# Kernel optimization log

Hardware: AMD Instinct MI355X
Metric: run time of the kernel (lower is better)

## Reference

```python
import jax, jax.numpy as jnp
import numpy as np

ALPHA = 20.0 / 100.0  # dt / tau
ONE_MINUS_ALPHA = 1.0 - ALPHA


def setup_inputs() -> dict:
    key = jax.random.key(0)
    ks = jax.random.split(key, 5)
    seq_len, batch, input_size, hidden_size = 512, 256, 64, 256
    x = jax.random.normal(ks[0], (seq_len, batch, input_size), dtype=jnp.float32)
    hidden = jnp.zeros((batch, hidden_size), dtype=jnp.float32)
    # per-step noise, shape (seq_len, hidden_size); broadcast over batch like torch.normal(std*ones(H))
    noise_seq = jax.random.normal(ks[1], (seq_len, hidden_size), dtype=jnp.float32)
    # small init scale keeps the leaky-relu recurrence stable over 512 steps
    W_in = jax.random.normal(ks[2], (hidden_size, input_size), dtype=jnp.float32) * 0.05
    b_in = jnp.zeros((hidden_size,), dtype=jnp.float32)
    W_hh = jax.random.normal(ks[3], (hidden_size, hidden_size), dtype=jnp.float32) * 0.05
    b_hh = jnp.zeros((hidden_size,), dtype=jnp.float32)
    return {"x": x, "hidden": hidden, "noise_seq": noise_seq,
            "W_in": W_in, "b_in": b_in, "W_hh": W_hh, "b_hh": b_hh}


def reference(x, hidden, noise_seq, W_in, b_in, W_hh, b_hh):
    # x: [T, B, I]; hidden: [B, H]; noise_seq: [T, H]
    def step(h, inp):
        xt, nt = inp  # xt: [B, I], nt: [H]
        pre = xt @ W_in.T + b_in + h @ W_hh.T + b_hh + nt
        h_new = jnp.maximum(h * ONE_MINUS_ALPHA + pre * ALPHA, 0.0)
        return h_new, h_new
    h_last, out = jax.lax.scan(step, hidden, (x, noise_seq))
    return out, h_last  # out: [T, B, H]
```

## Files before the change

### kernel.cpp

```cpp
#include <hip/hip_runtime.h>


#define T_STEPS 512
#define BATCH   256
#define INSZ    64
#define HID     256
#define ALPHA_F 0.2f
#define OMA_F   0.8f

__global__ __launch_bounds__(512, 2)
void ctrnn_prex(const float* __restrict__ x,
                const float* __restrict__ noise,
                const float* __restrict__ W_in,
                const float* __restrict__ b_in,
                const float* __restrict__ b_hh,
                float* __restrict__ prex)
{
    const int tid = threadIdx.x;
    const int j   = tid & (HID - 1);
    const int g   = tid >> 8;

    __shared__ __align__(16) float xs[2][2][INSZ];

    float win[INSZ];
#pragma unroll
    for (int k = 0; k < INSZ; k += 4) {
        float4 v = *reinterpret_cast<const float4*>(&W_in[j * INSZ + k]);
        win[k] = v.x; win[k+1] = v.y; win[k+2] = v.z; win[k+3] = v.w;
    }
    const float bias = b_in[j] + b_hh[j];

    const int base = blockIdx.x * 256;
    if (j < INSZ / 4) {
        *reinterpret_cast<float4*>(&xs[0][g][4 * j]) =
            *reinterpret_cast<const float4*>(&x[(size_t)(base + g) * INSZ + 4 * j]);
    }
    __syncthreads();

    int cur = 0;
#pragma unroll 1
    for (int i = 0; i < 128; ++i) {
        const int p = base + 2 * i + g;
        if (i + 1 < 128 && j < INSZ / 4) {
            *reinterpret_cast<float4*>(&xs[cur ^ 1][g][4 * j]) =
                *reinterpret_cast<const float4*>(
                    &x[(size_t)(p + 2) * INSZ + 4 * j]);
        }
        const int t = p >> 8;
        const float nz = noise[t * HID + j];

        float a0 = 0.f, a1 = 0.f, a2 = 0.f, a3 = 0.f;
#pragma unroll
        for (int k = 0; k < INSZ; k += 4) {
            float4 xv = *reinterpret_cast<const float4*>(&xs[cur][g][k]);
            a0 = fmaf(win[k],     xv.x, a0);
            a1 = fmaf(win[k + 1], xv.y, a1);
            a2 = fmaf(win[k + 2], xv.z, a2);
            a3 = fmaf(win[k + 3], xv.w, a3);
        }
        prex[(size_t)p * HID + j] = (a0 + a1) + (a2 + a3) + bias + nz;
        __syncthreads();
        cur ^= 1;
    }
}

__global__ __launch_bounds__(1024, 4)
void ctrnn_rec(const float* __restrict__ hidden,
               const float* __restrict__ prex,
               const float* __restrict__ W_hh,
               float* __restrict__ out)
{
    const int tid = threadIdx.x;
    const int jj  = tid & 63;
    const int g   = tid >> 6;
    const int b   = blockIdx.x;

    __shared__ __align__(16) float hbuf[2][HID];
    __shared__ __align__(16) float pbuf[16][HID];

    float w[4][16];
#pragma unroll
    for (int m = 0; m < 4; ++m) {
        const float* wrow = &W_hh[(jj + 64 * m) * HID + 16 * g];
#pragma unroll
        for (int c = 0; c < 4; ++c) {
            float4 v = *reinterpret_cast<const float4*>(&wrow[4 * c]);
            w[m][4*c]   = v.x; w[m][4*c+1] = v.y;
            w[m][4*c+2] = v.z; w[m][4*c+3] = v.w;
        }
    }

    float hj = 0.f, pcur = 0.f, pn1 = 0.f;
    if (tid < HID) {
        hj = hidden[b * HID + tid];
        hbuf[0][tid] = hj;
        pcur = prex[(size_t)b * HID + tid];
        pn1  = prex[((size_t)1 * BATCH + b) * HID + tid];
    }
    __syncthreads();

    const int koff = 16 * g;
    int cur = 0;
#pragma unroll 1
    for (int t = 0; t < T_STEPS; ++t) {
        float pn2 = 0.f;
        if (tid < HID && t + 2 < T_STEPS) {
            pn2 = prex[((size_t)(t + 2) * BATCH + b) * HID + tid];
        }

        float4 h0 = *reinterpret_cast<const float4*>(&hbuf[cur][koff]);
        float4 h1 = *reinterpret_cast<const float4*>(&hbuf[cur][koff + 4]);
        float4 h2 = *reinterpret_cast<const float4*>(&hbuf[cur][koff + 8]);
        float4 h3 = *reinterpret_cast<const float4*>(&hbuf[cur][koff + 12]);

        float acc[4];
#pragma unroll
        for (int m = 0; m < 4; ++m) {
            float a = 0.f, bq = 0.f;
            a  = fmaf(w[m][0],  h0.x, a);  bq = fmaf(w[m][1],  h0.y, bq);
            a  = fmaf(w[m][2],  h0.z, a);  bq = fmaf(w[m][3],  h0.w, bq);
            a  = fmaf(w[m][4],  h1.x, a);  bq = fmaf(w[m][5],  h1.y, bq);
            a  = fmaf(w[m][6],  h1.z, a);  bq = fmaf(w[m][7],  h1.w, bq);
            a  = fmaf(w[m][8],  h2.x, a);  bq = fmaf(w[m][9],  h2.y, bq);
            a  = fmaf(w[m][10], h2.z, a);  bq = fmaf(w[m][11], h2.w, bq);
            a  = fmaf(w[m][12], h3.x, a);  bq = fmaf(w[m][13], h3.y, bq);
            a  = fmaf(w[m][14], h3.z, a);  bq = fmaf(w[m][15], h3.w, bq);
            acc[m] = a + bq;
        }
        pbuf[g][jj]       = acc[0];
        pbuf[g][jj + 64]  = acc[1];
        pbuf[g][jj + 128] = acc[2];
        pbuf[g][jj + 192] = acc[3];
        __syncthreads();

        const int nxt = cur ^ 1;
        if (tid < HID) {
            float s = pcur;
#pragma unroll
            for (int gg = 0; gg < 16; ++gg) s += pbuf[gg][tid];
            hj = fmaxf(fmaf(OMA_F, hj, ALPHA_F * s), 0.f);
            out[((size_t)t * BATCH + b) * HID + tid] = hj;
            hbuf[nxt][tid] = hj;
            pcur = pn1; pn1 = pn2;
        }
        __syncthreads();
        cur = nxt;
    }

    if (tid < HID) {
        out[(size_t)T_STEPS * BATCH * HID + (size_t)b * HID + tid] = hj;
    }
}

__global__ __launch_bounds__(512, 2)
void ctrnn_mono(const float* __restrict__ x, const float* __restrict__ hidden,
                const float* __restrict__ noise, const float* __restrict__ W_in,
                const float* __restrict__ b_in, const float* __restrict__ W_hh,
                const float* __restrict__ b_hh, float* __restrict__ out)
{
    const int tid  = threadIdx.x;
    const int j    = tid & (HID - 1);
    const int half = tid >> 8;
    const int b    = blockIdx.x;

    __shared__ __align__(16) float hbuf[2][HID];
    __shared__ __align__(16) float xbuf[2][INSZ];
    __shared__ __align__(16) float pbuf[HID];

    float whh[128];
    const float* wrow = &W_hh[j * HID + half * 128];
#pragma unroll
    for (int k = 0; k < 128; k += 4) {
        float4 v = *reinterpret_cast<const float4*>(&wrow[k]);
        whh[k] = v.x; whh[k+1] = v.y; whh[k+2] = v.z; whh[k+3] = v.w;
    }
    float win[32];
    const float* wirow = &W_in[j * INSZ + half * 32];
#pragma unroll
    for (int k = 0; k < 32; k += 4) {
        float4 v = *reinterpret_cast<const float4*>(&wirow[k]);
        win[k] = v.x; win[k+1] = v.y; win[k+2] = v.z; win[k+3] = v.w;
    }

    float bias = 0.f, hj = 0.f, noise_j = 0.f;
    if (half == 0) {
        bias = b_in[j] + b_hh[j];
        hj = hidden[b * HID + j];
        hbuf[0][j] = hj;
        noise_j = noise[j];
        if (j < INSZ / 4) {
            *reinterpret_cast<float4*>(&xbuf[0][4 * j]) =
                *reinterpret_cast<const float4*>(&x[(size_t)b * INSZ + 4 * j]);
        }
    }
    __syncthreads();

    const int hoff = half * 128;
    const int ioff = half * 32;
    int cur = 0;
#pragma unroll 1
    for (int t = 0; t < T_STEPS; ++t) {
        float4 xnext = make_float4(0.f, 0.f, 0.f, 0.f);
        float  nnext = 0.f;
        if (half == 1) {
            if (j < INSZ / 4 && t + 1 < T_STEPS) {
                xnext = *reinterpret_cast<const float4*>(
                    &x[((size_t)(t + 1) * BATCH + b) * INSZ + 4 * j]);
            }
        } else if (t + 1 < T_STEPS) {
            nnext = noise[(t + 1) * HID + j];
        }

        float a0 = 0.f, a1 = 0.f, a2 = 0.f, a3 = 0.f;
#pragma unroll
        for (int k = 0; k < 128; k += 4) {
            float4 hv = *reinterpret_cast<const float4*>(&hbuf[cur][hoff + k]);
            a0 = fmaf(whh[k],     hv.x, a0);
            a1 = fmaf(whh[k + 1], hv.y, a1);
            a2 = fmaf(whh[k + 2], hv.z, a2);
            a3 = fmaf(whh[k + 3], hv.w, a3);
        }
#pragma unroll
        for (int k = 0; k < 32; k += 4) {
            float4 xv = *reinterpret_cast<const float4*>(&xbuf[cur][ioff + k]);
            a0 = fmaf(win[k],     xv.x, a0);
            a1 = fmaf(win[k + 1], xv.y, a1);
            a2 = fmaf(win[k + 2], xv.z, a2);
            a3 = fmaf(win[k + 3], xv.w, a3);
        }
        const float acc = (a0 + a1) + (a2 + a3);

        if (half == 1) pbuf[j] = acc;
        __syncthreads();

        const int nxt = cur ^ 1;
        if (half == 0) {
            const float pre = acc + pbuf[j] + bias + noise_j;
            hj = fmaxf(fmaf(OMA_F, hj, ALPHA_F * pre), 0.f);
            out[((size_t)t * BATCH + b) * HID + j] = hj;
            hbuf[nxt][j] = hj;
            noise_j = nnext;
        } else if (j < INSZ / 4 && t + 1 < T_STEPS) {
            *reinterpret_cast<float4*>(&xbuf[nxt][4 * j]) = xnext;
        }
        __syncthreads();
        cur = nxt;
    }

    if (half == 0) {
        out[(size_t)T_STEPS * BATCH * HID + (size_t)b * HID + j] = hj;
    }
}

extern "C" void kernel_launch(void* const* d_in, const int* in_sizes, int n_in,
                              void* d_out, int out_size, void* d_ws, size_t ws_size,
                              hipStream_t stream) {
    const float* x      = (const float*)d_in[0];
    const float* hidden = (const float*)d_in[1];
    const float* noise  = (const float*)d_in[2];
    const float* W_in   = (const float*)d_in[3];
    const float* b_in   = (const float*)d_in[4];
    const float* W_hh   = (const float*)d_in[5];
    const float* b_hh   = (const float*)d_in[6];
    float* out = (float*)d_out;

    const size_t prex_bytes = (size_t)T_STEPS * BATCH * HID * sizeof(float);
    if (ws_size >= prex_bytes) {
        float* prex = (float*)d_ws;
        hipLaunchKernelGGL(ctrnn_prex, dim3(512), dim3(512), 0, stream,
                           x, noise, W_in, b_in, b_hh, prex);
        hipLaunchKernelGGL(ctrnn_rec, dim3(BATCH), dim3(1024), 0, stream,
                           hidden, prex, W_hh, out);
    } else {
        hipLaunchKernelGGL(ctrnn_mono, dim3(BATCH), dim3(512), 0, stream,
                           x, hidden, noise, W_in, b_in, W_hh, b_hh, out);
    }
}
```

Baseline: 613.4 us.

## Fuse input projection into recurrent kernel with single barrier per step

Drops the separate input-projection kernel and its 128MB workspace round trip, folding the W_in·x product into the per-step recurrent matvec. Each 16-wide group handles 4 input columns alongside its W_hh slice. The reduction is spread across all threads with shuffles, and the partial-sum buffer is double-buffered so each timestep needs one raw s_barrier instead of two __syncthreads. The hidden-state buffer is now single, and its correctness depends on barrier ordering. That adds more per-step work inside the serial loop in exchange for removing global memory traffic.

```diff
diff --git a/kernel.cpp b/kernel.cpp
--- a/kernel.cpp
+++ b/kernel.cpp
@@ -8,247 +8,124 @@
 #define ALPHA_F 0.2f
 #define OMA_F   0.8f
 
-__global__ __launch_bounds__(512, 2)
-void ctrnn_prex(const float* __restrict__ x,
-                const float* __restrict__ noise,
-                const float* __restrict__ W_in,
-                const float* __restrict__ b_in,
-                const float* __restrict__ b_hh,
-                float* __restrict__ prex)
+__global__ __launch_bounds__(1024, 4)
+void ctrnn_fused(const float* __restrict__ x,
+                 const float* __restrict__ hidden,
+                 const float* __restrict__ noise,
+                 const float* __restrict__ W_in,
+                 const float* __restrict__ b_in,
+                 const float* __restrict__ W_hh,
+                 const float* __restrict__ b_hh,
+                 float* __restrict__ out)
 {
-    const int tid = threadIdx.x;
-    const int j   = tid & (HID - 1);
-    const int g   = tid >> 8;
+    const int tid  = threadIdx.x;
+    const int lane = tid & 63;
+    const int g    = tid >> 6;
+    const int b    = blockIdx.x;
 
-    __shared__ __align__(16) float xs[2][2][INSZ];
-
-    float win[INSZ];
-#pragma unroll
-    for (int k = 0; k < INSZ; k += 4) {
-        float4 v = *reinterpret_cast<const float4*>(&W_in[j * INSZ + k]);
-        win[k] = v.x; win[k+1] = v.y; win[k+2] = v.z; win[k+3] = v.w;
-    }
-    const float bias = b_in[j] + b_hh[j];
-
-    const int base = blockIdx.x * 256;
-    if (j < INSZ / 4) {
-        *reinterpret_cast<float4*>(&xs[0][g][4 * j]) =
-            *reinterpret_cast<const float4*>(&x[(size_t)(base + g) * INSZ + 4 * j]);
-    }
-    __syncthreads();
-
-    int cur = 0;
-#pragma unroll 1
-    for (int i = 0; i < 128; ++i) {
-        const int p = base + 2 * i + g;
-        if (i + 1 < 128 && j < INSZ / 4) {
-            *reinterpret_cast<float4*>(&xs[cur ^ 1][g][4 * j]) =
-                *reinterpret_cast<const float4*>(
-                    &x[(size_t)(p + 2) * INSZ + 4 * j]);
-        }
-        const int t = p >> 8;
-        const float nz = noise[t * HID + j];
-
-        float a0 = 0.f, a1 = 0.f, a2 = 0.f, a3 = 0.f;
-#pragma unroll
-        for (int k = 0; k < INSZ; k += 4) {
-            float4 xv = *reinterpret_cast<const float4*>(&xs[cur][g][k]);
-            a0 = fmaf(win[k],     xv.x, a0);
-            a1 = fmaf(win[k + 1], xv.y, a1);
-            a2 = fmaf(win[k + 2], xv.z, a2);
-            a3 = fmaf(win[k + 3], xv.w, a3);
-        }
-        prex[(size_t)p * HID + j] = (a0 + a1) + (a2 + a3) + bias + nz;
-        __syncthreads();
-        cur ^= 1;
-    }
-}
-
-__global__ __launch_bounds__(1024, 4)
-void ctrnn_rec(const float* __restrict__ hidden,
-               const float* __restrict__ prex,
-               const float* __restrict__ W_hh,
-               float* __restrict__ out)
-{
-    const int tid = threadIdx.x;
-    const int jj  = tid & 63;
-    const int g   = tid >> 6;
-    const int b   = blockIdx.x;
-
-    __shared__ __align__(16) float hbuf[2][HID];
-    __shared__ __align__(16) float pbuf[16][HID];
+    __shared__ __align__(16) float xbuf[2][INSZ];
+    __shared__ __align__(16) float hbuf[HID];
+    __shared__ __align__(16) float pbuf[2][16 * 264];
 
     float w[4][16];
 #pragma unroll
     for (int m = 0; m < 4; ++m) {
-        const float* wrow = &W_hh[(jj + 64 * m) * HID + 16 * g];
+        const float* wr = &W_hh[(lane + 64 * m) * HID + 16 * g];
 #pragma unroll
         for (int c = 0; c < 4; ++c) {
-            float4 v = *reinterpret_cast<const float4*>(&wrow[4 * c]);
+            float4 v = *reinterpret_cast<const float4*>(&wr[4 * c]);
             w[m][4*c]   = v.x; w[m][4*c+1] = v.y;
             w[m][4*c+2] = v.z; w[m][4*c+3] = v.w;
         }
     }
+    float wi[4][4];
+#pragma unroll
+    for (int m = 0; m < 4; ++m) {
+        float4 v = *reinterpret_cast<const float4*>(
+            &W_in[(lane + 64 * m) * INSZ + 4 * g]);
+        wi[m][0] = v.x; wi[m][1] = v.y; wi[m][2] = v.z; wi[m][3] = v.w;
+    }
 
-    float hj = 0.f, pcur = 0.f, pn1 = 0.f;
-    if (tid < HID) {
-        hj = hidden[b * HID + tid];
-        hbuf[0][tid] = hj;
-        pcur = prex[(size_t)b * HID + tid];
-        pn1  = prex[((size_t)1 * BATCH + b) * HID + tid];
+    const int rrow = 16 * g + (lane & 15);
+    const float biasl = b_in[rrow] + b_hh[rrow];
+    float hj  = hidden[b * HID + rrow];
+    float nn0 = noise[rrow];
+    float nn1 = noise[HID + rrow];
+
+    float4 xr = make_float4(0.f, 0.f, 0.f, 0.f);
+    if (g == 0 && lane < 16) {
+        *reinterpret_cast<float4*>(&xbuf[0][4 * lane]) =
+            *reinterpret_cast<const float4*>(&x[(size_t)b * INSZ + 4 * lane]);
+        xr = *reinterpret_cast<const float4*>(
+            &x[((size_t)BATCH + b) * INSZ + 4 * lane]);
     }
+    if (lane < 16) hbuf[rrow] = hj;
     __syncthreads();
 
-    const int koff = 16 * g;
-    int cur = 0;
+    const int redoff = ((g >> 2) << 6) + ((g & 3) << 4) + (lane & 15);
+    const int q = lane >> 4;
+
 #pragma unroll 1
     for (int t = 0; t < T_STEPS; ++t) {
-        float pn2 = 0.f;
-        if (tid < HID && t + 2 < T_STEPS) {
-            pn2 = prex[((size_t)(t + 2) * BATCH + b) * HID + tid];
+        const int cur = t & 1;
+
+        float nn2 = 0.f;
+        if (t + 2 < T_STEPS) nn2 = noise[(t + 2) * HID + rrow];
+        if (g == 0 && lane < 16) {
+            *reinterpret_cast<float4*>(&xbuf[cur ^ 1][4 * lane]) = xr;
+            if (t + 2 < T_STEPS)
+                xr = *reinterpret_cast<const float4*>(
+                    &x[((size_t)(t + 2) * BATCH + b) * INSZ + 4 * lane]);
         }
 
-        float4 h0 = *reinterpret_cast<const float4*>(&hbuf[cur][koff]);
-        float4 h1 = *reinterpret_cast<const float4*>(&hbuf[cur][koff + 4]);
-        float4 h2 = *reinterpret_cast<const float4*>(&hbuf[cur][koff + 8]);
-        float4 h3 = *reinterpret_cast<const float4*>(&hbuf[cur][koff + 12]);
+        const float4 h0 = *reinterpret_cast<const float4*>(&hbuf[16 * g]);
+        const float4 h1 = *reinterpret_cast<const float4*>(&hbuf[16 * g + 4]);
+        const float4 h2 = *reinterpret_cast<const float4*>(&hbuf[16 * g + 8]);
+        const float4 h3 = *reinterpret_cast<const float4*>(&hbuf[16 * g + 12]);
+        const float4 xv = *reinterpret_cast<const float4*>(&xbuf[cur][4 * g]);
 
-        float acc[4];
+        float accs[4];
 #pragma unroll
         for (int m = 0; m < 4; ++m) {
-            float a = 0.f, bq = 0.f;
-            a  = fmaf(w[m][0],  h0.x, a);  bq = fmaf(w[m][1],  h0.y, bq);
+            float a  = w[m][0] * h0.x;
+            float bq = w[m][1] * h0.y;
+            float cc = wi[m][0] * xv.x;
+            float dd = wi[m][1] * xv.y;
             a  = fmaf(w[m][2],  h0.z, a);  bq = fmaf(w[m][3],  h0.w, bq);
+            cc = fmaf(wi[m][2], xv.z, cc); dd = fmaf(wi[m][3], xv.w, dd);
             a  = fmaf(w[m][4],  h1.x, a);  bq = fmaf(w[m][5],  h1.y, bq);
             a  = fmaf(w[m][6],  h1.z, a);  bq = fmaf(w[m][7],  h1.w, bq);
             a  = fmaf(w[m][8],  h2.x, a);  bq = fmaf(w[m][9],  h2.y, bq);
             a  = fmaf(w[m][10], h2.z, a);  bq = fmaf(w[m][11], h2.w, bq);
             a  = fmaf(w[m][12], h3.x, a);  bq = fmaf(w[m][13], h3.y, bq);
             a  = fmaf(w[m][14], h3.z, a);  bq = fmaf(w[m][15], h3.w, bq);
-            acc[m] = a + bq;
+            accs[m] = (a + bq) + (cc + dd);
         }
-        pbuf[g][jj]       = acc[0];
-        pbuf[g][jj + 64]  = acc[1];
-        pbuf[g][jj + 128] = acc[2];
-        pbuf[g][jj + 192] = acc[3];
-        __syncthreads();
 
-        const int nxt = cur ^ 1;
-        if (tid < HID) {
-            float s = pcur;
-#pragma unroll
-            for (int gg = 0; gg < 16; ++gg) s += pbuf[gg][tid];
-            hj = fmaxf(fmaf(OMA_F, hj, ALPHA_F * s), 0.f);
-            out[((size_t)t * BATCH + b) * HID + tid] = hj;
-            hbuf[nxt][tid] = hj;
-            pcur = pn1; pn1 = pn2;
+        float* pb = &pbuf[cur][g * 264 + lane];
+        pb[0]   = accs[0];
+        pb[64]  = accs[1];
+        pb[128] = accs[2];
+        pb[192] = accs[3];
+
+        asm volatile("s_waitcnt lgkmcnt(0)\n\ts_barrier" ::: "memory");
+
+        const float* pr = &pbuf[cur][q * 264 + redoff];
+        float s = (pr[0] + pr[1056]) + (pr[2112] + pr[3168]);
+        s += __shfl_xor(s, 16);
+        s += __shfl_xor(s, 32);
+
+        const float pre = s + biasl + nn0;
+        hj = fmaxf(fmaf(OMA_F, hj, ALPHA_F * pre), 0.f);
+        if (lane < 16) {
+            out[((size_t)t * BATCH + b) * HID + rrow] = hj;
+            hbuf[rrow] = hj;
         }
-        __syncthreads();
-        cur = nxt;
+        nn0 = nn1; nn1 = nn2;
     }
 
-    if (tid < HID) {
-        out[(size_t)T_STEPS * BATCH * HID + (size_t)b * HID + tid] = hj;
-    }
-}
-
-__global__ __launch_bounds__(512, 2)
-void ctrnn_mono(const float* __restrict__ x, const float* __restrict__ hidden,
-                const float* __restrict__ noise, const float* __restrict__ W_in,
-                const float* __restrict__ b_in, const float* __restrict__ W_hh,
-                const float* __restrict__ b_hh, float* __restrict__ out)
-{
-    const int tid  = threadIdx.x;
-    const int j    = tid & (HID - 1);
-    const int half = tid >> 8;
-    const int b    = blockIdx.x;
-
-    __shared__ __align__(16) float hbuf[2][HID];
-    __shared__ __align__(16) float xbuf[2][INSZ];
-    __shared__ __align__(16) float pbuf[HID];
-
-    float whh[128];
-    const float* wrow = &W_hh[j * HID + half * 128];
-#pragma unroll
-    for (int k = 0; k < 128; k += 4) {
-        float4 v = *reinterpret_cast<const float4*>(&wrow[k]);
-        whh[k] = v.x; whh[k+1] = v.y; whh[k+2] = v.z; whh[k+3] = v.w;
-    }
-    float win[32];
-    const float* wirow = &W_in[j * INSZ + half * 32];
-#pragma unroll
-    for (int k = 0; k < 32; k += 4) {
-        float4 v = *reinterpret_cast<const float4*>(&wirow[k]);
-        win[k] = v.x; win[k+1] = v.y; win[k+2] = v.z; win[k+3] = v.w;
-    }
-
-    float bias = 0.f, hj = 0.f, noise_j = 0.f;
-    if (half == 0) {
-        bias = b_in[j] + b_hh[j];
-        hj = hidden[b * HID + j];
-        hbuf[0][j] = hj;
-        noise_j = noise[j];
-        if (j < INSZ / 4) {
-            *reinterpret_cast<float4*>(&xbuf[0][4 * j]) =
-                *reinterpret_cast<const float4*>(&x[(size_t)b * INSZ + 4 * j]);
-        }
-    }
-    __syncthreads();
-
-    const int hoff = half * 128;
-    const int ioff = half * 32;
-    int cur = 0;
-#pragma unroll 1
-    for (int t = 0; t < T_STEPS; ++t) {
-        float4 xnext = make_float4(0.f, 0.f, 0.f, 0.f);
-        float  nnext = 0.f;
-        if (half == 1) {
-            if (j < INSZ / 4 && t + 1 < T_STEPS) {
-                xnext = *reinterpret_cast<const float4*>(
-                    &x[((size_t)(t + 1) * BATCH + b) * INSZ + 4 * j]);
-            }
-        } else if (t + 1 < T_STEPS) {
-            nnext = noise[(t + 1) * HID + j];
-        }
-
-        float a0 = 0.f, a1 = 0.f, a2 = 0.f, a3 = 0.f;
-#pragma unroll
-        for (int k = 0; k < 128; k += 4) {
-            float4 hv = *reinterpret_cast<const float4*>(&hbuf[cur][hoff + k]);
-            a0 = fmaf(whh[k],     hv.x, a0);
-            a1 = fmaf(whh[k + 1], hv.y, a1);
-            a2 = fmaf(whh[k + 2], hv.z, a2);
-            a3 = fmaf(whh[k + 3], hv.w, a3);
-        }
-#pragma unroll
-        for (int k = 0; k < 32; k += 4) {
-            float4 xv = *reinterpret_cast<const float4*>(&xbuf[cur][ioff + k]);
-            a0 = fmaf(win[k],     xv.x, a0);
-            a1 = fmaf(win[k + 1], xv.y, a1);
-            a2 = fmaf(win[k + 2], xv.z, a2);
-            a3 = fmaf(win[k + 3], xv.w, a3);
-        }
-        const float acc = (a0 + a1) + (a2 + a3);
-
-        if (half == 1) pbuf[j] = acc;
-        __syncthreads();
-
-        const int nxt = cur ^ 1;
-        if (half == 0) {
-            const float pre = acc + pbuf[j] + bias + noise_j;
-            hj = fmaxf(fmaf(OMA_F, hj, ALPHA_F * pre), 0.f);
-            out[((size_t)t * BATCH + b) * HID + j] = hj;
-            hbuf[nxt][j] = hj;
-            noise_j = nnext;
-        } else if (j < INSZ / 4 && t + 1 < T_STEPS) {
-            *reinterpret_cast<float4*>(&xbuf[nxt][4 * j]) = xnext;
-        }
-        __syncthreads();
-        cur = nxt;
-    }
-
-    if (half == 0) {
-        out[(size_t)T_STEPS * BATCH * HID + (size_t)b * HID + j] = hj;
+    if (lane < 16) {
+        out[(size_t)T_STEPS * BATCH * HID + (size_t)b * HID + rrow] = hj;
     }
 }
 
@@ -264,15 +141,6 @@
     const float* b_hh   = (const float*)d_in[6];
     float* out = (float*)d_out;
 
-    const size_t prex_bytes = (size_t)T_STEPS * BATCH * HID * sizeof(float);
-    if (ws_size >= prex_bytes) {
-        float* prex = (float*)d_ws;
-        hipLaunchKernelGGL(ctrnn_prex, dim3(512), dim3(512), 0, stream,
-                           x, noise, W_in, b_in, b_hh, prex);
-        hipLaunchKernelGGL(ctrnn_rec, dim3(BATCH), dim3(1024), 0, stream,
-                           hidden, prex, W_hh, out);
-    } else {
-        hipLaunchKernelGGL(ctrnn_mono, dim3(BATCH), dim3(512), 0, stream,
-                           x, hidden, noise, W_in, b_in, W_hh, b_hh, out);
-    }
+    hipLaunchKernelGGL(ctrnn_fused, dim3(BATCH), dim3(1024), 0, stream,
+                       x, hidden, noise, W_in, b_in, W_hh, b_hh, out);
 }
```

Result: slower. 809.8 us (+32.0%).

## Halve per-step barriers in recurrence and tile the input projection over more rows

Applied to the files above, without the earlier changes.

The recurrent kernel now has every warp redundantly reduce the partial sums for its own 16 hidden rows, using strided shared-memory loads and cross-lane shuffles. Because each warp then reads back only the rows it wrote, the hidden state needs no second barrier. Partial sums are double-buffered and padded, leaving one barrier per timestep. The input-projection kernel now processes 128 rows per block with staged 32-row x tiles and folds the noise into the bias. The trade is extra redundant shared-memory reads and reduction work per warp, and an inline-asm barrier whose correctness depends on the buffering.

```diff
diff --git a/kernel.cpp b/kernel.cpp
--- a/kernel.cpp
+++ b/kernel.cpp
@@ -8,116 +8,129 @@
 #define ALPHA_F 0.2f
 #define OMA_F   0.8f
 
-__global__ __launch_bounds__(512, 2)
-void ctrnn_prex(const float* __restrict__ x,
-                const float* __restrict__ noise,
-                const float* __restrict__ W_in,
-                const float* __restrict__ b_in,
-                const float* __restrict__ b_hh,
-                float* __restrict__ prex)
+__global__ __launch_bounds__(256, 4)
+void ctrnn_prex2(const float* __restrict__ x,
+                 const float* __restrict__ noise,
+                 const float* __restrict__ W_in,
+                 const float* __restrict__ b_in,
+                 const float* __restrict__ b_hh,
+                 float* __restrict__ prex)
 {
-    const int tid = threadIdx.x;
-    const int j   = tid & (HID - 1);
-    const int g   = tid >> 8;
-
-    __shared__ __align__(16) float xs[2][2][INSZ];
-
-    float win[INSZ];
+    const int j  = threadIdx.x;
+    const int bb = blockIdx.x;
+    const int p0 = bb * 128;
+    const int t  = p0 >> 8;
+
+    __shared__ __align__(16) float xs[2][32][INSZ];
+
+    float w[INSZ];
 #pragma unroll
     for (int k = 0; k < INSZ; k += 4) {
         float4 v = *reinterpret_cast<const float4*>(&W_in[j * INSZ + k]);
-        win[k] = v.x; win[k+1] = v.y; win[k+2] = v.z; win[k+3] = v.w;
-    }
-    const float bias = b_in[j] + b_hh[j];
-
-    const int base = blockIdx.x * 256;
-    if (j < INSZ / 4) {
-        *reinterpret_cast<float4*>(&xs[0][g][4 * j]) =
-            *reinterpret_cast<const float4*>(&x[(size_t)(base + g) * INSZ + 4 * j]);
+        w[k] = v.x; w[k+1] = v.y; w[k+2] = v.z; w[k+3] = v.w;
+    }
+    const float bias = b_in[j] + b_hh[j] + noise[t * HID + j];
+
+    {
+        const float4* s4 = reinterpret_cast<const float4*>(&x[(size_t)p0 * INSZ]);
+        float4* d4 = reinterpret_cast<float4*>(&xs[0][0][0]);
+        d4[j] = s4[j]; d4[j + 256] = s4[j + 256];
     }
     __syncthreads();
 
-    int cur = 0;
 #pragma unroll 1
-    for (int i = 0; i < 128; ++i) {
-        const int p = base + 2 * i + g;
-        if (i + 1 < 128 && j < INSZ / 4) {
-            *reinterpret_cast<float4*>(&xs[cur ^ 1][g][4 * j]) =
-                *reinterpret_cast<const float4*>(
-                    &x[(size_t)(p + 2) * INSZ + 4 * j]);
-        }
-        const int t = p >> 8;
-        const float nz = noise[t * HID + j];
-
-        float a0 = 0.f, a1 = 0.f, a2 = 0.f, a3 = 0.f;
-#pragma unroll
-        for (int k = 0; k < INSZ; k += 4) {
-            float4 xv = *reinterpret_cast<const float4*>(&xs[cur][g][k]);
-            a0 = fmaf(win[k],     xv.x, a0);
-            a1 = fmaf(win[k + 1], xv.y, a1);
-            a2 = fmaf(win[k + 2], xv.z, a2);
-            a3 = fmaf(win[k + 3], xv.w, a3);
-        }
-        prex[(size_t)p * HID + j] = (a0 + a1) + (a2 + a3) + bias + nz;
+    for (int c = 0; c < 4; ++c) {
+        const int cur = c & 1;
+
+        float4 st0 = make_float4(0.f,0.f,0.f,0.f), st1 = st0;
+        if (c < 3) {
+            const float4* s4 = reinterpret_cast<const float4*>(
+                &x[(size_t)(p0 + (c + 1) * 32) * INSZ]);
+            st0 = s4[j]; st1 = s4[j + 256];
+        }
+
+        float* op = &prex[(size_t)(p0 + c * 32) * HID + j];
+#pragma unroll 2
+        for (int pp = 0; pp < 32; ++pp) {
+            float a0 = 0.f, a1 = 0.f, a2 = 0.f, a3 = 0.f;
+#pragma unroll
+            for (int k = 0; k < INSZ; k += 4) {
+                float4 xv = *reinterpret_cast<const float4*>(&xs[cur][pp][k]);
+                a0 = fmaf(w[k],     xv.x, a0);
+                a1 = fmaf(w[k + 1], xv.y, a1);
+                a2 = fmaf(w[k + 2], xv.z, a2);
+                a3 = fmaf(w[k + 3], xv.w, a3);
+            }
+            op[(size_t)pp * HID] = (a0 + a1) + (a2 + a3) + bias;
+        }
+
+        if (c < 3) {
+            float4* d4 = reinterpret_cast<float4*>(&xs[cur ^ 1][0][0]);
+            d4[j] = st0; d4[j + 256] = st1;
+        }
         __syncthreads();
-        cur ^= 1;
     }
 }
 
 __global__ __launch_bounds__(1024, 4)
-void ctrnn_rec(const float* __restrict__ hidden,
-               const float* __restrict__ prex,
-               const float* __restrict__ W_hh,
-               float* __restrict__ out)
+void ctrnn_rec2(const float* __restrict__ hidden,
+                const float* __restrict__ prex,
+                const float* __restrict__ W_hh,
+                float* __restrict__ out)
 {
-    const int tid = threadIdx.x;
-    const int jj  = tid & 63;
-    const int g   = tid >> 6;
-    const int b   = blockIdx.x;
-
-    __shared__ __align__(16) float hbuf[2][HID];
-    __shared__ __align__(16) float pbuf[16][HID];
+    const int tid  = threadIdx.x;
+    const int lane = tid & 63;
+    const int g    = tid >> 6;
+    const int b    = blockIdx.x;
+
+    __shared__ __align__(16) float hbuf[HID];
+    __shared__ __align__(16) float pbuf[2][16 * 264];
 
     float w[4][16];
 #pragma unroll
     for (int m = 0; m < 4; ++m) {
-        const float* wrow = &W_hh[(jj + 64 * m) * HID + 16 * g];
+        const float* wr = &W_hh[(lane + 64 * m) * HID + 16 * g];
 #pragma unroll
         for (int c = 0; c < 4; ++c) {
-            float4 v = *reinterpret_cast<const float4*>(&wrow[4 * c]);
+            float4 v = *reinterpret_cast<const float4*>(&wr[4 * c]);
             w[m][4*c]   = v.x; w[m][4*c+1] = v.y;
             w[m][4*c+2] = v.z; w[m][4*c+3] = v.w;
         }
     }
 
-    float hj = 0.f, pcur = 0.f, pn1 = 0.f;
-    if (tid < HID) {
-        hj = hidden[b * HID + tid];
-        hbuf[0][tid] = hj;
-        pcur = prex[(size_t)b * HID + tid];
-        pn1  = prex[((size_t)1 * BATCH + b) * HID + tid];
-    }
+    const int rrow = 16 * g + (lane & 15);
+    float hj = hidden[b * HID + rrow];
+
+    const float* pp = &prex[(size_t)b * HID + rrow];
+    float pcur = pp[0];
+    float pn1  = pp[BATCH * HID];
+    pp += 2 * (size_t)BATCH * HID;
+    float* op = &out[(size_t)b * HID + rrow];
+
+    if (lane < 16) hbuf[rrow] = hj;
     __syncthreads();
 
-    const int koff = 16 * g;
-    int cur = 0;
+    const int redoff = ((g >> 2) << 6) + ((g & 3) << 4) + (lane & 15);
+    const int q = lane >> 4;
+
 #pragma unroll 1
     for (int t = 0; t < T_STEPS; ++t) {
+        const int cur = t & 1;
+
         float pn2 = 0.f;
-        if (tid < HID && t + 2 < T_STEPS) {
-            pn2 = prex[((size_t)(t + 2) * BATCH + b) * HID + tid];
-        }
-
-        float4 h0 = *reinterpret_cast<const float4*>(&hbuf[cur][koff]);
-        float4 h1 = *reinterpret_cast<const float4*>(&hbuf[cur][koff + 4]);
-        float4 h2 = *reinterpret_cast<const float4*>(&hbuf[cur][koff + 8]);
-        float4 h3 = *reinterpret_cast<const float4*>(&hbuf[cur][koff + 12]);
-
-        float acc[4];
+        if (t + 2 < T_STEPS) pn2 = pp[0];
+        pp += (size_t)BATCH * HID;
+
+        const float4 h0 = *reinterpret_cast<const float4*>(&hbuf[16 * g]);
+        const float4 h1 = *reinterpret_cast<const float4*>(&hbuf[16 * g + 4]);
+        const float4 h2 = *reinterpret_cast<const float4*>(&hbuf[16 * g + 8]);
+        const float4 h3 = *reinterpret_cast<const float4*>(&hbuf[16 * g + 12]);
+
+        float accs[4];
 #pragma unroll
         for (int m = 0; m < 4; ++m) {
-            float a = 0.f, bq = 0.f;
-            a  = fmaf(w[m][0],  h0.x, a);  bq = fmaf(w[m][1],  h0.y, bq);
+            float a  = w[m][0] * h0.x;
+            float bq = w[m][1] * h0.y;
             a  = fmaf(w[m][2],  h0.z, a);  bq = fmaf(w[m][3],  h0.w, bq);
             a  = fmaf(w[m][4],  h1.x, a);  bq = fmaf(w[m][5],  h1.y, bq);
             a  = fmaf(w[m][6],  h1.z, a);  bq = fmaf(w[m][7],  h1.w, bq);
@@ -125,30 +138,33 @@
             a  = fmaf(w[m][10], h2.z, a);  bq = fmaf(w[m][11], h2.w, bq);
             a  = fmaf(w[m][12], h3.x, a);  bq = fmaf(w[m][13], h3.y, bq);
             a  = fmaf(w[m][14], h3.z, a);  bq = fmaf(w[m][15], h3.w, bq);
-            acc[m] = a + bq;
-        }
-        pbuf[g][jj]       = acc[0];
-        pbuf[g][jj + 64]  = acc[1];
-        pbuf[g][jj + 128] = acc[2];
-        pbuf[g][jj + 192] = acc[3];
-        __syncthreads();
-
-        const int nxt = cur ^ 1;
-        if (tid < HID) {
-            float s = pcur;
-#pragma unroll
-            for (int gg = 0; gg < 16; ++gg) s += pbuf[gg][tid];
-            hj = fmaxf(fmaf(OMA_F, hj, ALPHA_F * s), 0.f);
-            out[((size_t)t * BATCH + b) * HID + tid] = hj;
-            hbuf[nxt][tid] = hj;
-            pcur = pn1; pn1 = pn2;
-        }
-        __syncthreads();
-        cur = nxt;
-    }
-
-    if (tid < HID) {
-        out[(size_t)T_STEPS * BATCH * HID + (size_t)b * HID + tid] = hj;
+            accs[m] = a + bq;
+        }
+
+        float* pb = &pbuf[cur][g * 264 + lane];
+        pb[0]   = accs[0];
+        pb[64]  = accs[1];
+        pb[128] = accs[2];
+        pb[192] = accs[3];
+
+        asm volatile("s_waitcnt lgkmcnt(0)\n\ts_barrier" ::: "memory");
+
+        const float* pr = &pbuf[cur][q * 264 + redoff];
+        float s = (pr[0] + pr[1056]) + (pr[2112] + pr[3168]);
+        s += __shfl_xor(s, 16);
+        s += __shfl_xor(s, 32);
+
+        hj = fmaxf(fmaf(OMA_F, hj, ALPHA_F * (s + pcur)), 0.f);
+        if (lane < 16) {
+            op[0] = hj;
+            hbuf[rrow] = hj;
+        }
+        op += (size_t)BATCH * HID;
+        pcur = pn1; pn1 = pn2;
+    }
+
+    if (lane < 16) {
+        out[(size_t)T_STEPS * BATCH * HID + (size_t)b * HID + rrow] = hj;
     }
 }
 
@@ -267,9 +283,9 @@
     const size_t prex_bytes = (size_t)T_STEPS * BATCH * HID * sizeof(float);
     if (ws_size >= prex_bytes) {
         float* prex = (float*)d_ws;
-        hipLaunchKernelGGL(ctrnn_prex, dim3(512), dim3(512), 0, stream,
+        hipLaunchKernelGGL(ctrnn_prex2, dim3(1024), dim3(256), 0, stream,
                            x, noise, W_in, b_in, b_hh, prex);
-        hipLaunchKernelGGL(ctrnn_rec, dim3(BATCH), dim3(1024), 0, stream,
+        hipLaunchKernelGGL(ctrnn_rec2, dim3(BATCH), dim3(1024), 0, stream,
                            hidden, prex, W_hh, out);
     } else {
         hipLaunchKernelGGL(ctrnn_mono, dim3(BATCH), dim3(512), 0, stream,
```

New measurement: 1.471 ms. +139.8%, slower.

## Restructure input projection kernel to stage 32 rows per sync and split K across half-waves

Applied to the files above, without the earlier changes.

The pre-activation kernel now loads 32 input rows into shared memory per barrier instead of 2, cutting the barrier count from 128 to 8 per block. Each column's 64-wide dot product is split between two half-waves with a shuffle reduction, so each thread keeps 32 weights in registers instead of 64. Noise is folded into the per-thread bias once, since each block covers exactly one timestep. In exchange, half the lanes sit idle at the store and a cross-lane shuffle is added for every output row.

```diff
diff --git a/kernel.cpp b/kernel.cpp
--- a/kernel.cpp
+++ b/kernel.cpp
@@ -9,58 +9,75 @@
 #define OMA_F   0.8f
 
 __global__ __launch_bounds__(512, 2)
-void ctrnn_prex(const float* __restrict__ x,
-                const float* __restrict__ noise,
-                const float* __restrict__ W_in,
-                const float* __restrict__ b_in,
-                const float* __restrict__ b_hh,
-                float* __restrict__ prex)
+void ctrnn_prex3(const float* __restrict__ x,
+                 const float* __restrict__ noise,
+                 const float* __restrict__ W_in,
+                 const float* __restrict__ b_in,
+                 const float* __restrict__ b_hh,
+                 float* __restrict__ prex)
 {
-    const int tid = threadIdx.x;
-    const int j   = tid & (HID - 1);
-    const int g   = tid >> 8;
-
-    __shared__ __align__(16) float xs[2][2][INSZ];
-
-    float win[INSZ];
-#pragma unroll
-    for (int k = 0; k < INSZ; k += 4) {
-        float4 v = *reinterpret_cast<const float4*>(&W_in[j * INSZ + k]);
-        win[k] = v.x; win[k+1] = v.y; win[k+2] = v.z; win[k+3] = v.w;
-    }
-    const float bias = b_in[j] + b_hh[j];
-
-    const int base = blockIdx.x * 256;
-    if (j < INSZ / 4) {
-        *reinterpret_cast<float4*>(&xs[0][g][4 * j]) =
-            *reinterpret_cast<const float4*>(&x[(size_t)(base + g) * INSZ + 4 * j]);
+    const int tid  = threadIdx.x;
+    const int lane = tid & 63;
+    const int wv   = tid >> 6;
+    const int cl   = lane & 31;
+    const int hf   = lane >> 5;
+    const int col  = wv * 32 + cl;
+    const int bb   = blockIdx.x;
+    const int p0   = bb * 256;
+
+    __shared__ __align__(16) float xs[2][32][INSZ];
+
+    float w[32];
+    {
+        const float* wr = &W_in[col * INSZ + hf * 32];
+#pragma unroll
+        for (int k = 0; k < 32; k += 4) {
+            float4 v = *reinterpret_cast<const float4*>(&wr[k]);
+            w[k] = v.x; w[k+1] = v.y; w[k+2] = v.z; w[k+3] = v.w;
+        }
+    }
+    const float bias = b_in[col] + b_hh[col] + noise[bb * HID + col];
+
+    {
+        const float4* s4 = reinterpret_cast<const float4*>(&x[(size_t)p0 * INSZ]);
+        reinterpret_cast<float4*>(&xs[0][0][0])[tid] = s4[tid];
     }
     __syncthreads();
 
-    int cur = 0;
+    const int khf = hf * 32;
 #pragma unroll 1
-    for (int i = 0; i < 128; ++i) {
-        const int p = base + 2 * i + g;
-        if (i + 1 < 128 && j < INSZ / 4) {
-            *reinterpret_cast<float4*>(&xs[cur ^ 1][g][4 * j]) =
-                *reinterpret_cast<const float4*>(
-                    &x[(size_t)(p + 2) * INSZ + 4 * j]);
-        }
-        const int t = p >> 8;
-        const float nz = noise[t * HID + j];
-
-        float a0 = 0.f, a1 = 0.f, a2 = 0.f, a3 = 0.f;
-#pragma unroll
-        for (int k = 0; k < INSZ; k += 4) {
-            float4 xv = *reinterpret_cast<const float4*>(&xs[cur][g][k]);
-            a0 = fmaf(win[k],     xv.x, a0);
-            a1 = fmaf(win[k + 1], xv.y, a1);
-            a2 = fmaf(win[k + 2], xv.z, a2);
-            a3 = fmaf(win[k + 3], xv.w, a3);
-        }
-        prex[(size_t)p * HID + j] = (a0 + a1) + (a2 + a3) + bias + nz;
-        __syncthreads();
-        cur ^= 1;
+    for (int c = 0; c < 8; ++c) {
+        const int cur = c & 1;
+
+        float4 st = make_float4(0.f, 0.f, 0.f, 0.f);
+        if (c < 7) {
+            st = reinterpret_cast<const float4*>(
+                &x[(size_t)(p0 + (c + 1) * 32) * INSZ])[tid];
+        }
+
+        float* op = &prex[(size_t)(p0 + c * 32) * HID + col];
+#pragma unroll 2
+        for (int pp = 0; pp < 32; ++pp) {
+            float a0 = 0.f, a1 = 0.f, a2 = 0.f, a3 = 0.f;
+#pragma unroll
+            for (int k = 0; k < 32; k += 4) {
+                float4 xv = *reinterpret_cast<const float4*>(&xs[cur][pp][khf + k]);
+                a0 = fmaf(w[k],     xv.x, a0);
+                a1 = fmaf(w[k + 1], xv.y, a1);
+                a2 = fmaf(w[k + 2], xv.z, a2);
+                a3 = fmaf(w[k + 3], xv.w, a3);
+            }
+            float s = (a0 + a1) + (a2 + a3);
+            s += __shfl_xor(s, 32);
+            if (hf == 0) {
+                op[(size_t)pp * HID] = s + bias;
+            }
+        }
+
+        if (c < 7) {
+            reinterpret_cast<float4*>(&xs[cur ^ 1][0][0])[tid] = st;
+        }
+        __syncthreads();
     }
 }
 
@@ -267,7 +284,7 @@
     const size_t prex_bytes = (size_t)T_STEPS * BATCH * HID * sizeof(float);
     if (ws_size >= prex_bytes) {
         float* prex = (float*)d_ws;
-        hipLaunchKernelGGL(ctrnn_prex, dim3(512), dim3(512), 0, stream,
+        hipLaunchKernelGGL(ctrnn_prex3, dim3(512), dim3(512), 0, stream,
                            x, noise, W_in, b_in, b_hh, prex);
         hipLaunchKernelGGL(ctrnn_rec, dim3(BATCH), dim3(1024), 0, stream,
                            hidden, prex, W_hh, out);
```

After: 557.3 us. 9.2% less time.
